# Performance work log

Measured on AMD Instinct MI355X. Metric: run time of the kernel, lower is better.

## Reference

```python
import jax, jax.numpy as jnp
import numpy as np
import math

K = 7
B, C, H, W = 16, 3, 256, 256
N = 50000
ANGLE = 30.0; TRANS = 0.45; SHEAR = 0.3; SCALE0, SCALE1 = 1.0, 0.5  # self.scale assumed [1.0,0.5] (upstream AutoDO)


def _bilinear(img, xs, ys):
    # img: (C,Hs,Ws); xs,ys: (Ho,Wo) pixel coords; border padding (clamp)
    Cc, Hs, Ws = img.shape
    xs = jnp.clip(xs, 0.0, Ws - 1.0)
    ys = jnp.clip(ys, 0.0, Hs - 1.0)
    x0 = jnp.floor(xs); y0 = jnp.floor(ys)
    wx = xs - x0; wy = ys - y0
    x0i = x0.astype(jnp.int32); y0i = y0.astype(jnp.int32)
    x1i = jnp.minimum(x0i + 1, Ws - 1); y1i = jnp.minimum(y0i + 1, Hs - 1)
    Ia = img[:, y0i, x0i]; Ib = img[:, y0i, x1i]
    Ic = img[:, y1i, x0i]; Id = img[:, y1i, x1i]
    return Ia * (1 - wx) * (1 - wy) + Ib * wx * (1 - wy) + Ic * (1 - wx) * wy + Id * wx * wy


def _resize(x, Ho, Wo):
    # torch F.interpolate bilinear, align_corners=False, no antialias
    Bb, Cc, Hs, Ws = x.shape
    ys = (jnp.arange(Ho, dtype=x.dtype) + 0.5) * (Hs / Ho) - 0.5
    xs = (jnp.arange(Wo, dtype=x.dtype) + 0.5) * (Ws / Wo) - 0.5
    Y, X = jnp.meshgrid(ys, xs, indexing='ij')
    return jax.vmap(lambda im: _bilinear(im, X, Y))(x)


def _warp_perspective(x, M, Ho, Wo):
    # kornia.warp_perspective: dst(p) = src(M^-1 p), bilinear, border padding, align_corners=True
    Bb, Cc, Hs, Ws = x.shape
    Minv = jnp.linalg.inv(M)  # (B,3,3)
    yy, xx = jnp.meshgrid(jnp.arange(Ho, dtype=x.dtype), jnp.arange(Wo, dtype=x.dtype), indexing='ij')
    pts = jnp.stack([xx.ravel(), yy.ravel(), jnp.ones(Ho * Wo, dtype=x.dtype)])  # (3, Ho*Wo)
    src = jnp.einsum('bij,jn->bin', Minv, pts)
    xs = (src[:, 0] / src[:, 2]).reshape(Bb, Ho, Wo)
    ys = (src[:, 1] / src[:, 2]).reshape(Bb, Ho, Wo)
    return jax.vmap(_bilinear)(x, xs, ys)


def _forward(x, paramP, paramM, gumbel_u, eps, idx):
    dt = x.dtype
    pP = jax.nn.sigmoid(paramP[:, idx])  # (K,B)
    logits = jnp.stack([jnp.log(pP).ravel(), jnp.log(1.0 - pP).ravel()], axis=1)  # (K*B,2)
    g = -jnp.log(-jnp.log(gumbel_u))
    y_soft = jax.nn.softmax(logits + g, axis=1)  # tau=1
    y_hard = jax.nn.one_hot(jnp.argmax(y_soft, axis=1), 2, dtype=y_soft.dtype)
    y = y_hard + y_soft - jax.lax.stop_gradient(y_soft)  # straight-through hard gumbel
    sP = y[:, 0].reshape(K, B)
    sM = jax.nn.sigmoid(paramM[:, idx]) * eps  # (K,B)
    ang = sP[0] * sM[0] * ANGLE
    # replicate torch's cat(W//2 * ones(B), H//2 * ones(B)).view(-1,2) layout exactly
    ctr = jnp.concatenate([jnp.full((B,), W // 2, dt), jnp.full((B,), H // 2, dt)]).reshape(-1, 2)
    sx = SCALE0 + sP[5] * sM[5] * SCALE1
    sy = SCALE0 + sP[6] * sM[6] * SCALE1
    rad = jnp.deg2rad(ang); ca = jnp.cos(rad); sa = jnp.sin(rad)
    # kornia get_rotation_matrix2d: rot=[[c,s],[-s,c]] @ diag(sx,sy); t = ctr - rot@ctr
    sr = jnp.stack([jnp.stack([ca * sx, sa * sy], -1), jnp.stack([-sa * sx, ca * sy], -1)], -2)  # (B,2,2)
    t = ctr - jnp.einsum('bij,bj->bi', sr, ctr)
    eye = jnp.broadcast_to(jnp.eye(3, dtype=dt), (B, 3, 3))
    R = eye.at[:, :2, :2].set(sr).at[:, :2, 2].set(t)
    T = eye.at[:, 0, 2].set(W * sP[1] * sM[1] * TRANS).at[:, 1, 2].set(H * sP[2] * sM[2] * TRANS)
    S = eye.at[:, 0, 1].set(sP[3] * sM[3] * SHEAR).at[:, 1, 0].set(sP[4] * sM[4] * SHEAR)
    M = S @ T @ R
    x_up = _resize(x, 4 * H, 4 * W)
    x_w = _warp_perspective(x_up, M, 4 * H, 4 * W)
    return _resize(x_w, H, W)


def setup_inputs() -> dict:
    key = jax.random.key(0)
    k1, k2, k3, k4 = jax.random.split(key, 4)
    p = 1.0 / (K - 2)
    prob_logit = math.log(p / (1.0 - p))
    m = 5.0 / 10.0
    magn_logit = math.log(m / (1.0 - m))
    return {
        'x': jax.random.uniform(k1, (B, C, H, W), jnp.float32),
        'paramP': jnp.full((K, N), prob_logit, jnp.float32),
        'paramM': jnp.full((K, N), magn_logit, jnp.float32),
        'gumbel_u': jax.random.uniform(k2, (K * B, 2), jnp.float32, minval=1e-6, maxval=1.0 - 1e-6),
        'eps': jax.random.normal(k3, (K, B), jnp.float32),
        'idx': jax.random.randint(k4, (B,), 0, N, jnp.int32),
    }


def reference(x, paramP, paramM, gumbel_u, eps, idx):
    return _forward(x, paramP, paramM, gumbel_u, eps, idx)
```

## Files before the change

### kernel.cpp

```cpp
#include <hip/hip_runtime.h>
#include <math.h>


typedef float floatx4 __attribute__((ext_vector_type(4)));

__device__ __forceinline__ floatx4 load4(const float* p) {
    floatx4 v;
    __builtin_memcpy(&v, p, sizeof(v));
    return v;
}

struct Up { int i0; float w; };

__device__ __forceinline__ Up upc(int v) {
    float u = fmaf(0.25f, (float)v, -0.375f);
    u = fminf(fmaxf(u, 0.0f), 255.0f);
    float f = floorf(u);
    Up r; r.i0 = (int)f; r.w = u - f;
    return r;
}

struct Trip { float w0, w1, w2; int base; };

__device__ __forceinline__ Trip merged3(float s) {
    float f = floorf(s);
    float fr = s - f;
    int v0 = (int)f;
    int v1 = min(v0 + 1, 1023);
    Up c0 = upc(v0), c1 = upc(v1);
    float A0 = 1.0f - fr, A1 = fr;
    float b0 = A1 * (1.0f - c1.w), b1 = A1 * c1.w;
    bool d = (c1.i0 != c0.i0);
    Trip t;
    t.w0 = A0 * (1.0f - c0.w) + (d ? 0.0f : b0);
    t.w1 = A0 * c0.w + (d ? b0 : b1);
    t.w2 = d ? b1 : 0.0f;
    t.base = c0.i0;
    return t;
}

__global__ __launch_bounds__(256) void fused_warp(
    const float* __restrict__ x,
    const float* __restrict__ paramP, const float* __restrict__ paramM,
    const float* __restrict__ gumbel_u, const float* __restrict__ eps,
    const int* __restrict__ idx,
    float* __restrict__ out, int N)
{
    __shared__ float smem[8];

    int b = blockIdx.z;
    int tid = threadIdx.y * 16 + threadIdx.x;

    if (tid < 64) {
        float dec = 0.f, sMv = 0.f;
        if (tid < 7) {
            int k = tid;
            int id = idx[b];
            float vP = paramP[k * N + id];
            float pP = 1.0f / (1.0f + expf(-vP));
            float l0 = logf(pP);
            float l1 = logf(1.0f - pP);
            float u0 = gumbel_u[(k * 16 + b) * 2 + 0];
            float u1 = gumbel_u[(k * 16 + b) * 2 + 1];
            float g0 = -logf(-logf(u0));
            float g1 = -logf(-logf(u1));
            dec = (l0 + g0 >= l1 + g1) ? 1.0f : 0.0f;
            float vM = paramM[k * N + id];
            float sig = 1.0f / (1.0f + expf(-vM));
            sMv = sig * eps[k * 16 + b];
        }
        float sP[7], sM[7];
#pragma unroll
        for (int k = 0; k < 7; ++k) {
            sP[k] = __shfl(dec, k, 64);
            sM[k] = __shfl(sMv, k, 64);
        }
        if (tid == 0) {
            float ang = sP[0] * sM[0] * 30.0f;
            float rad = ang * 0.017453292519943295f;
            float ca = cosf(rad), sa = sinf(rad);
            float sx = 1.0f + sP[5] * sM[5] * 0.5f;
            float sy = 1.0f + sP[6] * sM[6] * 0.5f;
            float sr00 = ca * sx, sr01 = sa * sy;
            float sr10 = -sa * sx, sr11 = ca * sy;
            float t0 = 128.0f - (sr00 + sr01) * 128.0f;
            float t1 = 128.0f - (sr10 + sr11) * 128.0f;
            float tx = 256.0f * sP[1] * sM[1] * 0.45f;
            float ty = 256.0f * sP[2] * sM[2] * 0.45f;
            float sh01 = sP[3] * sM[3] * 0.3f;
            float sh10 = sP[4] * sM[4] * 0.3f;
            float e0 = t0 + tx, e1 = t1 + ty;
            float a  = sr00 + sh01 * sr10;
            float bb = sr01 + sh01 * sr11;
            float txm = e0 + sh01 * e1;
            float c  = sh10 * sr00 + sr10;
            float d  = sh10 * sr01 + sr11;
            float tym = sh10 * e0 + e1;
            float det = a * d - bb * c;
            float rdet = 1.0f / det;
            smem[0] = d * rdet;
            smem[1] = -bb * rdet;
            smem[2] = (bb * tym - d * txm) * rdet;
            smem[3] = -c * rdet;
            smem[4] = a * rdet;
            smem[5] = (c * txm - a * tym) * rdet;
        }
    }
    __syncthreads();

    float m00 = smem[0], m01 = smem[1], m02 = smem[2];
    float m10 = smem[3], m11 = smem[4], m12 = smem[5];

    int j = blockIdx.x * 16 + threadIdx.x;
    int i = blockIdx.y * 16 + threadIdx.y;
    const float* xb = x + b * 3 * 65536;
    float acc[3] = {0.f, 0.f, 0.f};

#pragma unroll
    for (int p = 0; p < 2; ++p) {
        float XA = (float)(4 * j + 1);
        float Yp = (float)(4 * i + 1 + p);
        float xAu = fmaf(m00, XA, fmaf(m01, Yp, m02));
        float yAu = fmaf(m10, XA, fmaf(m11, Yp, m12));
        float xBu = xAu + m00;
        float yBu = yAu + m10;
        float xsA = fminf(fmaxf(xAu, 0.f), 1023.f);
        float ysA = fminf(fmaxf(yAu, 0.f), 1023.f);
        float xsB = fminf(fmaxf(xBu, 0.f), 1023.f);
        float ysB = fminf(fmaxf(yBu, 0.f), 1023.f);
        Trip cA = merged3(xsA), cB = merged3(xsB);
        Trip rA = merged3(ysA), rB = merged3(ysB);
        int cb = min(cA.base, cB.base);
        int rb = min(rA.base, rB.base);
        float CA[4], CB[4], RA[4], RB[4];
        bool sa_ = (cA.base != cb);
        CA[0] = sa_ ? 0.f : cA.w0;
        CA[1] = sa_ ? cA.w0 : cA.w1;
        CA[2] = sa_ ? cA.w1 : cA.w2;
        CA[3] = sa_ ? cA.w2 : 0.f;
        bool sb_ = (cB.base != cb);
        CB[0] = sb_ ? 0.f : cB.w0;
        CB[1] = sb_ ? cB.w0 : cB.w1;
        CB[2] = sb_ ? cB.w1 : cB.w2;
        CB[3] = sb_ ? cB.w2 : 0.f;
        bool ra_ = (rA.base != rb);
        RA[0] = ra_ ? 0.f : rA.w0;
        RA[1] = ra_ ? rA.w0 : rA.w1;
        RA[2] = ra_ ? rA.w1 : rA.w2;
        RA[3] = ra_ ? rA.w2 : 0.f;
        bool rb_ = (rB.base != rb);
        RB[0] = rb_ ? 0.f : rB.w0;
        RB[1] = rb_ ? rB.w0 : rB.w1;
        RB[2] = rb_ ? rB.w1 : rB.w2;
        RB[3] = rb_ ? rB.w2 : 0.f;

        float W[4][4];
#pragma unroll
        for (int r = 0; r < 4; ++r)
#pragma unroll
            for (int c = 0; c < 4; ++c)
                W[r][c] = fmaf(RB[r], CB[c], RA[r] * CA[c]);

        int base = cb;
        if (cb > 252) {
            int shift = cb - 252;
            base = 252;
            for (int s = 0; s < shift; ++s) {
#pragma unroll
                for (int r = 0; r < 4; ++r) {
                    W[r][3] = W[r][2];
                    W[r][2] = W[r][1];
                    W[r][1] = W[r][0];
                    W[r][0] = 0.f;
                }
            }
        }

        int e0 = rb * 256 + base;
        int e1 = min(rb + 1, 255) * 256 + base;
        int e2 = min(rb + 2, 255) * 256 + base;
        int e3 = min(rb + 3, 255) * 256 + base;

#pragma unroll
        for (int ch = 0; ch < 3; ++ch) {
            const float* pc = xb + ch * 65536;
            floatx4 L0 = load4(pc + e0);
            floatx4 L1 = load4(pc + e1);
            floatx4 L2 = load4(pc + e2);
            floatx4 L3 = load4(pc + e3);
            float s0 = fmaf(W[0][3], L0.w, fmaf(W[0][2], L0.z, fmaf(W[0][1], L0.y, W[0][0] * L0.x)));
            float s1 = fmaf(W[1][3], L1.w, fmaf(W[1][2], L1.z, fmaf(W[1][1], L1.y, W[1][0] * L1.x)));
            float s2 = fmaf(W[2][3], L2.w, fmaf(W[2][2], L2.z, fmaf(W[2][1], L2.y, W[2][0] * L2.x)));
            float s3 = fmaf(W[3][3], L3.w, fmaf(W[3][2], L3.z, fmaf(W[3][1], L3.y, W[3][0] * L3.x)));
            acc[ch] += (s0 + s1) + (s2 + s3);
        }
    }

    int obase = ((b * 3) * 256 + i) * 256 + j;
    out[obase]          = 0.25f * acc[0];
    out[obase + 65536]  = 0.25f * acc[1];
    out[obase + 131072] = 0.25f * acc[2];
}

extern "C" void kernel_launch(void* const* d_in, const int* in_sizes, int n_in,
                              void* d_out, int out_size, void* d_ws, size_t ws_size,
                              hipStream_t stream) {
    const float* x      = (const float*)d_in[0];
    const float* paramP = (const float*)d_in[1];
    const float* paramM = (const float*)d_in[2];
    const float* gumbel = (const float*)d_in[3];
    const float* eps    = (const float*)d_in[4];
    const int*   idx    = (const int*)d_in[5];
    float* out  = (float*)d_out;
    int N = in_sizes[1] / 7;

    hipLaunchKernelGGL(fused_warp, dim3(16, 16, 16), dim3(16, 16, 1), 0, stream,
                       x, paramP, paramM, gumbel, eps, idx, out, N);
}
```

Before: 88.75 us.

## Interleave input channels into workspace so bilinear gathers fetch contiguous pixels

Adds a pre-pass kernel that rewrites the planar input (B,C,H,W) into a channel-interleaved layout in the workspace. The warp kernel then reads each 4-pixel row footprint as three contiguous float4 loads covering all channels, instead of four-wide loads from three separate channel planes. The aim is to improve cache-line locality of the gather. In exchange it adds an extra launch and a full read plus write of the input through memory. The new loads are also no longer 16-byte aligned.

```diff
diff --git a/kernel.cpp b/kernel.cpp
--- a/kernel.cpp
+++ b/kernel.cpp
@@ -8,6 +8,22 @@
     floatx4 v;
     __builtin_memcpy(&v, p, sizeof(v));
     return v;
+}
+
+__global__ __launch_bounds__(256) void interleave(
+    const float* __restrict__ x, float* __restrict__ xi)
+{
+    int g = blockIdx.x * 256 + threadIdx.x;
+    int b = g >> 16;
+    int p = g & 65535;
+    const float* xb = x + b * 3 * 65536 + p;
+    float v0 = xb[0];
+    float v1 = xb[65536];
+    float v2 = xb[131072];
+    float* o = xi + (size_t)g * 3;
+    o[0] = v0;
+    o[1] = v1;
+    o[2] = v2;
 }
 
 struct Up { int i0; float w; };
@@ -40,7 +56,7 @@
 }
 
 __global__ __launch_bounds__(256) void fused_warp(
-    const float* __restrict__ x,
+    const float* __restrict__ xi,
     const float* __restrict__ paramP, const float* __restrict__ paramM,
     const float* __restrict__ gumbel_u, const float* __restrict__ eps,
     const int* __restrict__ idx,
@@ -113,7 +129,7 @@
 
     int j = blockIdx.x * 16 + threadIdx.x;
     int i = blockIdx.y * 16 + threadIdx.y;
-    const float* xb = x + b * 3 * 65536;
+    const float* xb = xi + (size_t)b * 3 * 65536;
     float acc[3] = {0.f, 0.f, 0.f};
 
 #pragma unroll
@@ -180,19 +196,17 @@
         int e1 = min(rb + 1, 255) * 256 + base;
         int e2 = min(rb + 2, 255) * 256 + base;
         int e3 = min(rb + 3, 255) * 256 + base;
-
-#pragma unroll
-        for (int ch = 0; ch < 3; ++ch) {
-            const float* pc = xb + ch * 65536;
-            floatx4 L0 = load4(pc + e0);
-            floatx4 L1 = load4(pc + e1);
-            floatx4 L2 = load4(pc + e2);
-            floatx4 L3 = load4(pc + e3);
-            float s0 = fmaf(W[0][3], L0.w, fmaf(W[0][2], L0.z, fmaf(W[0][1], L0.y, W[0][0] * L0.x)));
-            float s1 = fmaf(W[1][3], L1.w, fmaf(W[1][2], L1.z, fmaf(W[1][1], L1.y, W[1][0] * L1.x)));
-            float s2 = fmaf(W[2][3], L2.w, fmaf(W[2][2], L2.z, fmaf(W[2][1], L2.y, W[2][0] * L2.x)));
-            float s3 = fmaf(W[3][3], L3.w, fmaf(W[3][2], L3.z, fmaf(W[3][1], L3.y, W[3][0] * L3.x)));
-            acc[ch] += (s0 + s1) + (s2 + s3);
+        int q[4] = {e0 * 3, e1 * 3, e2 * 3, e3 * 3};
+
+#pragma unroll
+        for (int r = 0; r < 4; ++r) {
+            const float* pr = xb + q[r];
+            floatx4 v0 = load4(pr);
+            floatx4 v1 = load4(pr + 4);
+            floatx4 v2 = load4(pr + 8);
+            acc[0] += fmaf(W[r][3], v2.y, fmaf(W[r][2], v1.z, fmaf(W[r][1], v0.w, W[r][0] * v0.x)));
+            acc[1] += fmaf(W[r][3], v2.z, fmaf(W[r][2], v1.w, fmaf(W[r][1], v1.x, W[r][0] * v0.y)));
+            acc[2] += fmaf(W[r][3], v2.w, fmaf(W[r][2], v2.x, fmaf(W[r][1], v1.y, W[r][0] * v0.z)));
         }
     }
 
@@ -211,9 +225,11 @@
     const float* gumbel = (const float*)d_in[3];
     const float* eps    = (const float*)d_in[4];
     const int*   idx    = (const int*)d_in[5];
-    float* out  = (float*)d_out;
+    float* out = (float*)d_out;
+    float* xi  = (float*)d_ws;
     int N = in_sizes[1] / 7;
 
+    hipLaunchKernelGGL(interleave, dim3(4096), dim3(256), 0, stream, x, xi);
     hipLaunchKernelGGL(fused_warp, dim3(16, 16, 16), dim3(16, 16, 1), 0, stream,
-                       x, paramP, paramM, gumbel, eps, idx, out, N);
-}
+                       xi, paramP, paramM, gumbel, eps, idx, out, N);
+}
```

Result: slower. 95.83 us (+8.0%).

## Stage per-block source footprint in LDS before bilinear gathers

Applied to the files above, without the earlier changes.

Each block computes the bounding box of its warped source footprint from the four tile corners, then cooperatively copies that region of all three channels into shared memory when it fits in 6144 floats. The 16 taps per subsample are then read from LDS instead of as unaligned 4-wide global loads, with a fallback to the original global path for large footprints. This aims to cut redundant global and cache traffic, at the cost of an extra sync, 24KB of LDS per block (which can lower occupancy), scalar LDS reads that may hit bank conflicts, and divergent code size.

```diff
diff --git a/kernel.cpp b/kernel.cpp
--- a/kernel.cpp
+++ b/kernel.cpp
@@ -3,6 +3,8 @@
 
 
 typedef float floatx4 __attribute__((ext_vector_type(4)));
+
+#define LDS_FLOATS 6144
 
 __device__ __forceinline__ floatx4 load4(const float* p) {
     floatx4 v;
@@ -47,6 +49,7 @@
     float* __restrict__ out, int N)
 {
     __shared__ float smem[8];
+    __shared__ float lds[LDS_FLOATS];
 
     int b = blockIdx.z;
     int tid = threadIdx.y * 16 + threadIdx.x;
@@ -114,6 +117,48 @@
     int j = blockIdx.x * 16 + threadIdx.x;
     int i = blockIdx.y * 16 + threadIdx.y;
     const float* xb = x + b * 3 * 65536;
+
+    float X0 = (float)(4 * (blockIdx.x * 16) + 1), X1 = X0 + 61.0f;
+    float Y0 = (float)(4 * (blockIdx.y * 16) + 1), Y1 = Y0 + 61.0f;
+    float xmin = 1e30f, xmax = -1e30f, ymin = 1e30f, ymax = -1e30f;
+#pragma unroll
+    for (int cx = 0; cx < 2; ++cx)
+#pragma unroll
+        for (int cy = 0; cy < 2; ++cy) {
+            float Xc = cx ? X1 : X0;
+            float Yc = cy ? Y1 : Y0;
+            float xs = fmaf(m00, Xc, fmaf(m01, Yc, m02));
+            float ys = fmaf(m10, Xc, fmaf(m11, Yc, m12));
+            xmin = fminf(xmin, xs); xmax = fmaxf(xmax, xs);
+            ymin = fminf(ymin, ys); ymax = fmaxf(ymax, ys);
+        }
+    xmin = fminf(fmaxf(xmin, 0.f), 1023.f);
+    xmax = fminf(fmaxf(xmax, 0.f), 1023.f);
+    ymin = fminf(fmaxf(ymin, 0.f), 1023.f);
+    ymax = fminf(fmaxf(ymax, 0.f), 1023.f);
+    int cmin = min(max((int)floorf(fmaf(0.25f, xmin, -0.375f)) - 1, 0), 255);
+    int cmax = min(max((int)floorf(fmaf(0.25f, xmax, -0.375f)) + 4, 0), 255);
+    int rmin = min(max((int)floorf(fmaf(0.25f, ymin, -0.375f)) - 1, 0), 255);
+    int rmax = min(max((int)floorf(fmaf(0.25f, ymax, -0.375f)) + 4, 0), 255);
+    int Wd = cmax - cmin + 1;
+    int Hd = rmax - rmin + 1;
+    int HW = Hd * Wd;
+    bool use_lds = (3 * HW <= LDS_FLOATS);
+
+    if (use_lds) {
+        for (int ch = 0; ch < 3; ++ch) {
+            const float* pc = xb + ch * 65536;
+            float* lc = lds + ch * HW;
+            for (int rr = threadIdx.y; rr < Hd; rr += 16) {
+                const float* prow = pc + (rmin + rr) * 256 + cmin;
+                float* lrow = lc + rr * Wd;
+                for (int cc = threadIdx.x; cc < Wd; cc += 16)
+                    lrow[cc] = prow[cc];
+            }
+        }
+    }
+    __syncthreads();
+
     float acc[3] = {0.f, 0.f, 0.f};
 
 #pragma unroll
@@ -161,38 +206,56 @@
             for (int c = 0; c < 4; ++c)
                 W[r][c] = fmaf(RB[r], CB[c], RA[r] * CA[c]);
 
-        int base = cb;
-        if (cb > 252) {
-            int shift = cb - 252;
-            base = 252;
-            for (int s = 0; s < shift; ++s) {
-#pragma unroll
-                for (int r = 0; r < 4; ++r) {
-                    W[r][3] = W[r][2];
-                    W[r][2] = W[r][1];
-                    W[r][1] = W[r][0];
-                    W[r][0] = 0.f;
+        if (use_lds) {
+            int cl[4], ro[4];
+#pragma unroll
+            for (int k = 0; k < 4; ++k) {
+                int cgl = min(min(cb + k, 255), cmax);
+                cl[k] = cgl - cmin;
+                int rgl = min(min(rb + k, 255), rmax);
+                ro[k] = (rgl - rmin) * Wd;
+            }
+#pragma unroll
+            for (int ch = 0; ch < 3; ++ch) {
+                const float* lc = lds + ch * HW;
+                float s0 = fmaf(W[0][3], lc[ro[0] + cl[3]], fmaf(W[0][2], lc[ro[0] + cl[2]], fmaf(W[0][1], lc[ro[0] + cl[1]], W[0][0] * lc[ro[0] + cl[0]])));
+                float s1 = fmaf(W[1][3], lc[ro[1] + cl[3]], fmaf(W[1][2], lc[ro[1] + cl[2]], fmaf(W[1][1], lc[ro[1] + cl[1]], W[1][0] * lc[ro[1] + cl[0]])));
+                float s2 = fmaf(W[2][3], lc[ro[2] + cl[3]], fmaf(W[2][2], lc[ro[2] + cl[2]], fmaf(W[2][1], lc[ro[2] + cl[1]], W[2][0] * lc[ro[2] + cl[0]])));
+                float s3 = fmaf(W[3][3], lc[ro[3] + cl[3]], fmaf(W[3][2], lc[ro[3] + cl[2]], fmaf(W[3][1], lc[ro[3] + cl[1]], W[3][0] * lc[ro[3] + cl[0]])));
+                acc[ch] += (s0 + s1) + (s2 + s3);
+            }
+        } else {
+            int base = cb;
+            if (cb > 252) {
+                int shift = cb - 252;
+                base = 252;
+                for (int s = 0; s < shift; ++s) {
+#pragma unroll
+                    for (int r = 0; r < 4; ++r) {
+                        W[r][3] = W[r][2];
+                        W[r][2] = W[r][1];
+                        W[r][1] = W[r][0];
+                        W[r][0] = 0.f;
+                    }
                 }
             }
-        }
-
-        int e0 = rb * 256 + base;
-        int e1 = min(rb + 1, 255) * 256 + base;
-        int e2 = min(rb + 2, 255) * 256 + base;
-        int e3 = min(rb + 3, 255) * 256 + base;
-
-#pragma unroll
-        for (int ch = 0; ch < 3; ++ch) {
-            const float* pc = xb + ch * 65536;
-            floatx4 L0 = load4(pc + e0);
-            floatx4 L1 = load4(pc + e1);
-            floatx4 L2 = load4(pc + e2);
-            floatx4 L3 = load4(pc + e3);
-            float s0 = fmaf(W[0][3], L0.w, fmaf(W[0][2], L0.z, fmaf(W[0][1], L0.y, W[0][0] * L0.x)));
-            float s1 = fmaf(W[1][3], L1.w, fmaf(W[1][2], L1.z, fmaf(W[1][1], L1.y, W[1][0] * L1.x)));
-            float s2 = fmaf(W[2][3], L2.w, fmaf(W[2][2], L2.z, fmaf(W[2][1], L2.y, W[2][0] * L2.x)));
-            float s3 = fmaf(W[3][3], L3.w, fmaf(W[3][2], L3.z, fmaf(W[3][1], L3.y, W[3][0] * L3.x)));
-            acc[ch] += (s0 + s1) + (s2 + s3);
+            int e0 = rb * 256 + base;
+            int e1 = min(rb + 1, 255) * 256 + base;
+            int e2 = min(rb + 2, 255) * 256 + base;
+            int e3 = min(rb + 3, 255) * 256 + base;
+#pragma unroll
+            for (int ch = 0; ch < 3; ++ch) {
+                const float* pc = xb + ch * 65536;
+                floatx4 L0 = load4(pc + e0);
+                floatx4 L1 = load4(pc + e1);
+                floatx4 L2 = load4(pc + e2);
+                floatx4 L3 = load4(pc + e3);
+                float s0 = fmaf(W[0][3], L0.w, fmaf(W[0][2], L0.z, fmaf(W[0][1], L0.y, W[0][0] * L0.x)));
+                float s1 = fmaf(W[1][3], L1.w, fmaf(W[1][2], L1.z, fmaf(W[1][1], L1.y, W[1][0] * L1.x)));
+                float s2 = fmaf(W[2][3], L2.w, fmaf(W[2][2], L2.z, fmaf(W[2][1], L2.y, W[2][0] * L2.x)));
+                float s3 = fmaf(W[3][3], L3.w, fmaf(W[3][2], L3.z, fmaf(W[3][1], L3.y, W[3][0] * L3.x)));
+                acc[ch] += (s0 + s1) + (s2 + s3);
+            }
         }
     }
 
@@ -211,7 +274,7 @@
     const float* gumbel = (const float*)d_in[3];
     const float* eps    = (const float*)d_in[4];
     const int*   idx    = (const int*)d_in[5];
-    float* out  = (float*)d_out;
+    float* out = (float*)d_out;
     int N = in_sizes[1] / 7;
 
     hipLaunchKernelGGL(fused_warp, dim3(16, 16, 16), dim3(16, 16, 1), 0, stream,
```

Measured after the change: 103.1 us. 1.16x slower.
